# Performance work log

Measured on AMD Instinct MI355X. Metric: run time of the kernel, lower is better.

Reference implementation:

```python
import jax, jax.numpy as jnp
import numpy as np

LN_EPS = 1e-5      # torch nn.LayerNorm default
NORM_EPS = 1e-12   # torch F.normalize default
EPS = 1e-8         # loss eps


def layer_norm(x, gamma, beta):
    mu = x.mean(axis=-1, keepdims=True)
    var = x.var(axis=-1, keepdims=True)  # biased, matches torch LN
    return (x - mu) * jax.lax.rsqrt(var + LN_EPS) * gamma + beta


def l2norm(x):
    n = jnp.sqrt(jnp.sum(x * x, axis=-1, keepdims=True))
    return x / jnp.maximum(n, NORM_EPS)


def setup_inputs() -> dict:
    key = jax.random.key(0)
    k1, k2, k3 = jax.random.split(key, 3)
    N, B, L, D = 1024, 64, 197, 768
    text_features = jax.random.normal(k1, (N, D), dtype=jnp.float32)
    vision_tokens = jax.random.normal(k2, (B, L, D), dtype=jnp.float32)
    group_map = jnp.sort(jax.random.randint(k3, (N,), 0, B)).astype(jnp.int64)
    ln_gamma = jnp.ones((D,), dtype=jnp.float32)
    ln_beta = jnp.zeros((D,), dtype=jnp.float32)
    log_loss_temp = jnp.array([np.log(0.07)], dtype=jnp.float32)
    return {
        "text_features": text_features,
        "vision_tokens": vision_tokens,
        "group_map": group_map,
        "ln_gamma": ln_gamma,
        "ln_beta": ln_beta,
        "log_loss_temp": log_loss_temp,
    }


def reference(text_features, vision_tokens, group_map, ln_gamma, ln_beta, log_loss_temp):
    D = text_features.shape[-1]
    # shared LayerNorm on both modalities
    tf = layer_norm(text_features, ln_gamma, ln_beta)          # [N, D]
    vt = layer_norm(vision_tokens, ln_gamma, ln_beta)          # [B, L, D]

    # SimilarityLogit, sim_op='dot': scores / sqrt(D), softmax over tokens
    scores = jnp.einsum('nd,bld->bnl', tf, vt) / jnp.sqrt(jnp.float32(D))
    attn = jax.nn.softmax(scores, axis=-1)                     # [B, N, L]
    aggregated = jnp.einsum('bnl,bld->bnd', attn, vt)          # [B, N, D]

    qn = l2norm(tf)                                            # [N, D]
    an = l2norm(aggregated)                                    # [B, N, D]
    logits = jnp.einsum('nd,bnd->nb', qn, an)                  # [N, B] (== [B,N].T)

    # multi-positive NCE loss (row_sum=False, col_sum=False)
    temp = jnp.exp(log_loss_temp)[0]
    scaled = jnp.exp(logits / temp)                            # [N, B]
    N = scaled.shape[0]
    idx = jnp.arange(N)
    pos = scaled[idx, group_map]                               # [N]

    # row loss: pos / sum over images
    row_p = pos / (scaled.sum(axis=1) + EPS)
    row_loss = -jnp.log(row_p + EPS)

    # column loss: pos / (pos + sum of negatives in its column)
    neg_mask = jnp.ones_like(scaled).at[idx, group_map].set(0.0)
    sum_neg = (scaled * neg_mask).sum(axis=0)[group_map]       # [N]
    col_p = pos / (pos + sum_neg + EPS)
    col_loss = -jnp.log(col_p + EPS)

    return (row_loss.mean() + col_loss.mean()) / 2
```

## Files before the change

kernel.cpp:

```cpp
#include <hip/hip_runtime.h>
#include <hip/hip_bf16.h>
#include <math.h>

#define NN 1024
#define BB 64
#define LL 197
#define LP 256
#define LBV 13
#define DD 768

typedef __attribute__((ext_vector_type(8))) short short8;
typedef __attribute__((ext_vector_type(4))) float f32x4;

constexpr float LN_EPS = 1e-5f;
constexpr float NORM_EPS = 1e-12f;
constexpr float EPS = 1e-8f;

__device__ __forceinline__ float waveSum(float v) {
#pragma unroll
    for (int m = 32; m >= 1; m >>= 1) v += __shfl_xor(v, m, 64);
    return v;
}
__device__ __forceinline__ float grpSum(float v) {
#pragma unroll
    for (int m = 8; m >= 1; m >>= 1) v += __shfl_xor(v, m, 64);
    return v;
}
__device__ __forceinline__ float grpMax(float v) {
#pragma unroll
    for (int m = 8; m >= 1; m >>= 1) v = fmaxf(v, __shfl_xor(v, m, 64));
    return v;
}

__device__ __forceinline__ float bf2f(unsigned short u) {
    unsigned int x = ((unsigned int)u) << 16;
    return reinterpret_cast<float&>(x);
}

__device__ __forceinline__ void gl_lds16(const void* g, void* l) {
    __builtin_amdgcn_global_load_lds(
        (const __attribute__((address_space(1))) unsigned int*)g,
        (__attribute__((address_space(3))) unsigned int*)l, 16, 0, 0);
}

__device__ __forceinline__ void lite_barrier() {
    asm volatile("s_barrier" ::: "memory");
}

__global__ __launch_bounds__(256) void ln_kernel(
    const float* __restrict__ x, __hip_bfloat16* __restrict__ y,
    const float* __restrict__ gamma, const float* __restrict__ beta,
    float* __restrict__ qinv) {
    const int row = blockIdx.x;
    const int tid = threadIdx.x;
    const float* xr = x + (size_t)row * DD;

    float v[3];
    float s = 0.f, ss = 0.f;
#pragma unroll
    for (int c = 0; c < 3; c++) {
        float t = xr[tid + 256 * c];
        v[c] = t; s += t; ss += t * t;
    }
    __shared__ float red[8];
    s = waveSum(s); ss = waveSum(ss);
    const int w = tid >> 6;
    if ((tid & 63) == 0) { red[w] = s; red[4 + w] = ss; }
    __syncthreads();
    s = red[0] + red[1] + red[2] + red[3];
    ss = red[4] + red[5] + red[6] + red[7];
    const float mean = s * (1.f / DD);
    const float var = ss * (1.f / DD) - mean * mean;
    const float rs = rsqrtf(var + LN_EPS);

    float q = 0.f;
#pragma unroll
    for (int c = 0; c < 3; c++) {
        const int d = tid + 256 * c;
        float t = (v[c] - mean) * rs * gamma[d] + beta[d];
        __hip_bfloat16 hb = __float2bfloat16(t);
        y[((size_t)(d >> 5) * NN + row) * 32 + (d & 31)] = hb;
        float tb = __bfloat162float(hb);
        q += tb * tb;
    }
    __syncthreads();
    q = waveSum(q);
    if ((tid & 63) == 0) red[w] = q;
    __syncthreads();
    if (tid == 0) {
        float n2 = red[0] + red[1] + red[2] + red[3];
        qinv[row] = 1.f / fmaxf(sqrtf(n2), NORM_EPS);
    }
}

__global__ __launch_bounds__(256) void ln_vis_kernel(
    const float* __restrict__ x, __hip_bfloat16* __restrict__ y,
    const float* __restrict__ gamma, const float* __restrict__ beta) {
    const int id = blockIdx.x;
    const int xcd = id & 7;
    const int k = id >> 3;
    const int bhi = k >> 8;
    const int l = k & 255;
    const int b = xcd + 8 * bhi;
    const int tid = threadIdx.x;
    if (l >= LL) {
#pragma unroll
        for (int c = 0; c < 3; c++) {
            const int d = tid + 256 * c;
            y[(((size_t)b * 24 + (d >> 5)) * LP + l) * 32 + (d & 31)] = __float2bfloat16(0.f);
        }
        return;
    }
    const float* xr = x + ((size_t)b * LL + l) * DD;

    float v[3];
    float s = 0.f, ss = 0.f;
#pragma unroll
    for (int c = 0; c < 3; c++) {
        float t = xr[tid + 256 * c];
        v[c] = t; s += t; ss += t * t;
    }
    __shared__ float red[8];
    s = waveSum(s); ss = waveSum(ss);
    const int w = tid >> 6;
    if ((tid & 63) == 0) { red[w] = s; red[4 + w] = ss; }
    __syncthreads();
    s = red[0] + red[1] + red[2] + red[3];
    ss = red[4] + red[5] + red[6] + red[7];
    const float mean = s * (1.f / DD);
    const float var = ss * (1.f / DD) - mean * mean;
    const float rs = rsqrtf(var + LN_EPS);
#pragma unroll
    for (int c = 0; c < 3; c++) {
        const int d = tid + 256 * c;
        y[(((size_t)b * 24 + (d >> 5)) * LP + l) * 32 + (d & 31)] =
            __float2bfloat16((v[c] - mean) * rs * gamma[d] + beta[d]);
    }
}

__global__ __launch_bounds__(256, 2) void gram_kernel(
    const __hip_bfloat16* __restrict__ vt_t, __hip_bfloat16* __restrict__ G_t) {
    const int id = blockIdx.x;
    const int xcd = id & 7;
    const int k = id >> 3;
    const int bhi = k >> 3;
    const int rb = k & 7;
    const int b = xcd + 8 * bhi;
    const int n0 = rb * 32;
    const int tid = threadIdx.x, w = tid >> 6, lane = tid & 63;
    const int g = lane >> 4, c = lane & 15;
    const int gsw = (g ^ ((c ^ (c >> 2)) & 3)) * 16;

    __shared__ __align__(16) unsigned char smem[49152];
    const char* vtbc = (const char*)vt_t + (size_t)b * 24 * 16384;

#define GSTAGE(ks, bsel)                                                        \
    {                                                                           \
        const char* vsl_ = vtbc + (size_t)(ks) * 16384;                         \
        _Pragma("unroll")                                                       \
        for (int q_ = 0; q_ < 4; q_++) {                                        \
            const int o_ = q_ * 4096 + tid * 16;                                \
            const int r_ = o_ >> 6;                                             \
            const int sj_ = ((o_ >> 4) & 3) ^ ((r_ ^ (r_ >> 2)) & 3);           \
            gl_lds16(vsl_ + r_ * 64 + sj_ * 16,                                 \
                     smem + (bsel) * 16384 + q_ * 4096 + w * 1024);             \
        }                                                                       \
    }

    f32x4 acc[4][2];
#pragma unroll
    for (int i = 0; i < 4; i++)
#pragma unroll
        for (int nb = 0; nb < 2; nb++) acc[i][nb] = {0.f, 0.f, 0.f, 0.f};

    GSTAGE(0, 0);
    GSTAGE(1, 1);
    asm volatile("s_waitcnt vmcnt(4)" ::: "memory");
    lite_barrier();

    for (int ks = 0; ks < 24; ks++) {
        if (ks < 22) GSTAGE(ks + 2, (ks + 2) % 3);
        const unsigned char* vb = smem + (ks % 3) * 16384;
        short8 af[2], bf[4];
#pragma unroll
        for (int nb = 0; nb < 2; nb++)
            af[nb] = *(const short8*)(vb + (n0 + nb * 16 + c) * 64 + gsw);
#pragma unroll
        for (int i = 0; i < 4; i++)
            bf[i] = *(const short8*)(vb + ((w + 4 * i) * 16 + c) * 64 + gsw);
#pragma unroll
        for (int i = 0; i < 4; i++)
#pragma unroll
            for (int nb = 0; nb < 2; nb++)
                acc[i][nb] = __builtin_amdgcn_mfma_f32_16x16x32_bf16(
                    af[nb], bf[i], acc[i][nb], 0, 0, 0);
        if (ks < 22) asm volatile("s_waitcnt vmcnt(4)" ::: "memory");
        else         asm volatile("s_waitcnt vmcnt(0)" ::: "memory");
        lite_barrier();
    }
#undef GSTAGE

#pragma unroll
    for (int i = 0; i < 4; i++) {
        const int cw = w + 4 * i;
#pragma unroll
        for (int nb = 0; nb < 2; nb++)
#pragma unroll
            for (int r = 0; r < 4; r++)
                G_t[(((size_t)b * 8 + (cw >> 1)) * LP + n0 + nb * 16 + g * 4 + r) * 32 +
                    (cw & 1) * 16 + c] = __float2bfloat16(acc[i][nb][r]);
    }
}

__global__ __launch_bounds__(256, 3) void score_kernel(
    const __hip_bfloat16* __restrict__ tf_t, const __hip_bfloat16* __restrict__ vt_t,
    const float* __restrict__ qinv, __hip_bfloat16* __restrict__ P_t,
    float* __restrict__ numq) {
    const int id = blockIdx.x;
    const int xcd = id & 7;
    const int kk = id >> 3;
    const int bhi = kk >> 4;
    const int nt = kk & 15;
    const int b = xcd + 8 * bhi;
    const int n0 = nt * 64;
    const int tid = threadIdx.x, w = tid >> 6, lane = tid & 63;
    const int g = lane >> 4, c = lane & 15;
    const int gsw = (g ^ ((c ^ (c >> 2)) & 3)) * 16;

    __shared__ __align__(16) unsigned char smem[34816];
    float* mx = (float*)smem;
    float* sm = mx + 256;
    float* nm = sm + 256;

    const char* vtbc = (const char*)vt_t + (size_t)b * 24 * 16384;
    const char* tfc = (const char*)tf_t;

#define SSTAGE(ks, bsel)                                                        \
    {                                                                           \
        const char* vsl_ = vtbc + (size_t)(ks) * 16384;                         \
        const char* tsl_ = tfc + (size_t)(ks) * 65536 + (size_t)n0 * 64;        \
        _Pragma("unroll")                                                       \
        for (int q_ = 0; q_ < 3; q_++) {                                        \
            const int o_ = q_ * 4096 + tid * 16;                                \
            const int r_ = o_ >> 6;                                             \
            const int sj_ = ((o_ >> 4) & 3) ^ ((r_ ^ (r_ >> 2)) & 3);           \
            gl_lds16(vsl_ + r_ * 64 + sj_ * 16,                                 \
                     smem + (bsel) * 13312 + q_ * 4096 + w * 1024);             \
        }                                                                       \
        if (lane < 16) {                                                        \
            const int o_ = 12288 + (w * 16 + lane) * 16;                        \
            const int r_ = o_ >> 6;                                             \
            const int sj_ = ((o_ >> 4) & 3) ^ ((r_ ^ (r_ >> 2)) & 3);           \
            gl_lds16(vsl_ + r_ * 64 + sj_ * 16,                                 \
                     smem + (bsel) * 13312 + 12288 + w * 256);                  \
        }                                                                       \
        {                                                                       \
            const int o_ = tid * 16;                                            \
            const int r_ = o_ >> 6;                                             \
            const int sj_ = ((o_ >> 4) & 3) ^ ((r_ ^ (r_ >> 2)) & 3);           \
            gl_lds16(tsl_ + r_ * 64 + sj_ * 16,                                 \
                     smem + 26624 + (bsel) * 4096 + w * 1024);                  \
        }                                                                       \
    }

    f32x4 acc[4][4];
#pragma unroll
    for (int i = 0; i < 4; i++)
#pragma unroll
        for (int nb = 0; nb < 4; nb++) acc[i][nb] = {0.f, 0.f, 0.f, 0.f};

    SSTAGE(0, 0);
    SSTAGE(1, 1);
    asm volatile("s_waitcnt vmcnt(5)" ::: "memory");
    lite_barrier();

    for (int ks = 0; ks < 24; ks++) {
        const unsigned char* vb = smem + (ks & 1) * 13312;
        const unsigned char* tb = smem + 26624 + (ks & 1) * 4096;
        short8 af[4];
#pragma unroll
        for (int nb = 0; nb < 4; nb++)
            af[nb] = *(const short8*)(tb + (nb * 16 + c) * 64 + gsw);
#pragma unroll
        for (int i = 0; i < 4; i++) {
            const int lb = w + 4 * i;
            if (lb < LBV) {
                short8 bfv = *(const short8*)(vb + (lb * 16 + c) * 64 + gsw);
#pragma unroll
                for (int nb = 0; nb < 4; nb++)
                    acc[i][nb] = __builtin_amdgcn_mfma_f32_16x16x32_bf16(
                        af[nb], bfv, acc[i][nb], 0, 0, 0);
            }
        }
        lite_barrier();
        if (ks < 22) {
            SSTAGE(ks + 2, ks & 1);
            asm volatile("s_waitcnt vmcnt(5)" ::: "memory");
        } else {
            asm volatile("s_waitcnt vmcnt(0)" ::: "memory");
        }
        lite_barrier();
    }
#undef SSTAGE

    const float inv_sqrtD = 0.0360843918f;
    float mp[4][4];
#pragma unroll
    for (int nb = 0; nb < 4; nb++)
#pragma unroll
        for (int r = 0; r < 4; r++) mp[nb][r] = -1e30f;
#pragma unroll
    for (int i = 0; i < 4; i++) {
        const int l = (w + 4 * i) * 16 + c;
        if (l < LL) {
#pragma unroll
            for (int nb = 0; nb < 4; nb++)
#pragma unroll
                for (int r = 0; r < 4; r++) mp[nb][r] = fmaxf(mp[nb][r], acc[i][nb][r]);
        }
    }
#pragma unroll
    for (int nb = 0; nb < 4; nb++)
#pragma unroll
        for (int r = 0; r < 4; r++) mp[nb][r] = grpMax(mp[nb][r]);
    if (c == 0) {
#pragma unroll
        for (int nb = 0; nb < 4; nb++)
#pragma unroll
            for (int r = 0; r < 4; r++) mx[(nb * 16 + g * 4 + r) * 4 + w] = mp[nb][r];
    }
    __syncthreads();
    float mf[4][4];
#pragma unroll
    for (int nb = 0; nb < 4; nb++)
#pragma unroll
        for (int r = 0; r < 4; r++) {
            const int row = nb * 16 + g * 4 + r;
            mf[nb][r] = fmaxf(fmaxf(mx[row * 4 + 0], mx[row * 4 + 1]),
                              fmaxf(mx[row * 4 + 2], mx[row * 4 + 3]));
        }

    float sp[4][4], np[4][4];
#pragma unroll
    for (int nb = 0; nb < 4; nb++)
#pragma unroll
        for (int r = 0; r < 4; r++) { sp[nb][r] = 0.f; np[nb][r] = 0.f; }
#pragma unroll
    for (int i = 0; i < 4; i++) {
        const int l = (w + 4 * i) * 16 + c;
#pragma unroll
        for (int nb = 0; nb < 4; nb++)
#pragma unroll
            for (int r = 0; r < 4; r++) {
                const float raw = acc[i][nb][r];
                const float p = (l < LL) ? __expf((raw - mf[nb][r]) * inv_sqrtD) : 0.f;
                acc[i][nb][r] = p;
                sp[nb][r] += p;
                np[nb][r] += p * raw;
            }
    }
#pragma unroll
    for (int nb = 0; nb < 4; nb++)
#pragma unroll
        for (int r = 0; r < 4; r++) { sp[nb][r] = grpSum(sp[nb][r]); np[nb][r] = grpSum(np[nb][r]); }
    if (c == 0) {
#pragma unroll
        for (int nb = 0; nb < 4; nb++)
#pragma unroll
            for (int r = 0; r < 4; r++) {
                const int row = nb * 16 + g * 4 + r;
                sm[row * 4 + w] = sp[nb][r];
                nm[row * 4 + w] = np[nb][r];
            }
    }
    __syncthreads();

    float invs[4][4];
#pragma unroll
    for (int nb = 0; nb < 4; nb++)
#pragma unroll
        for (int r = 0; r < 4; r++) {
            const int row = nb * 16 + g * 4 + r;
            const float ssum = sm[row * 4 + 0] + sm[row * 4 + 1] + sm[row * 4 + 2] + sm[row * 4 + 3];
            invs[nb][r] = 1.f / ssum;
        }

#pragma unroll
    for (int i = 0; i < 4; i++) {
        const int lb = w + 4 * i;
#pragma unroll
        for (int nb = 0; nb < 4; nb++)
#pragma unroll
            for (int r = 0; r < 4; r++)
                P_t[(((size_t)b * 8 + (lb >> 1)) * NN + n0 + nb * 16 + g * 4 + r) * 32 +
                    (lb & 1) * 16 + c] = __float2bfloat16(acc[i][nb][r] * invs[nb][r]);
    }

    if (tid < 64) {
        const int row = tid;
        const int n = n0 + row;
        const float ssum = sm[row * 4 + 0] + sm[row * 4 + 1] + sm[row * 4 + 2] + sm[row * 4 + 3];
        const float nsum = nm[row * 4 + 0] + nm[row * 4 + 1] + nm[row * 4 + 2] + nm[row * 4 + 3];
        numq[(size_t)n * BB + b] = (nsum / ssum) * qinv[n];
    }
}

__global__ __launch_bounds__(256, 3) void den_kernel(
    const __hip_bfloat16* __restrict__ P_t, const __hip_bfloat16* __restrict__ G_t,
    const float* __restrict__ numq, float* __restrict__ logits) {
    const int id = blockIdx.x;
    const int xcd = id & 7;
    const int kk = id >> 3;
    const int bhi = kk >> 4;
    const int nt = kk & 15;
    const int b = xcd + 8 * bhi;
    const int n0 = nt * 64;
    const int tid = threadIdx.x, w = tid >> 6, lane = tid & 63;
    const int g = lane >> 4, c = lane & 15;
    const int gsw = (g ^ ((c ^ (c >> 2)) & 3)) * 16;

    __shared__ __align__(16) unsigned char smem[34816];
    float* mx = (float*)smem;

    const char* Gbc = (const char*)G_t + (size_t)b * 8 * 16384;
    const char* Pbc = (const char*)P_t + (size_t)b * 8 * 65536;

#define DSTAGE(ks, bsel)                                                        \
    {                                                                           \
        const char* vsl_ = Gbc + (size_t)(ks) * 16384;                          \
        const char* psl_ = Pbc + (size_t)(ks) * 65536 + (size_t)n0 * 64;        \
        _Pragma("unroll")                                                       \
        for (int q_ = 0; q_ < 3; q_++) {                                        \
            const int o_ = q_ * 4096 + tid * 16;                                \
            const int r_ = o_ >> 6;                                             \
            const int sj_ = ((o_ >> 4) & 3) ^ ((r_ ^ (r_ >> 2)) & 3);           \
            gl_lds16(vsl_ + r_ * 64 + sj_ * 16,                                 \
                     smem + (bsel) * 13312 + q_ * 4096 + w * 1024);             \
        }                                                                       \
        if (lane < 16) {                                                        \
            const int o_ = 12288 + (w * 16 + lane) * 16;                        \
            const int r_ = o_ >> 6;                                             \
            const int sj_ = ((o_ >> 4) & 3) ^ ((r_ ^ (r_ >> 2)) & 3);           \
            gl_lds16(vsl_ + r_ * 64 + sj_ * 16,                                 \
                     smem + (bsel) * 13312 + 12288 + w * 256);                  \
        }                                                                       \
        {                                                                       \
            const int o_ = tid * 16;                                            \
            const int r_ = o_ >> 6;                                             \
            const int sj_ = ((o_ >> 4) & 3) ^ ((r_ ^ (r_ >> 2)) & 3);           \
            gl_lds16(psl_ + r_ * 64 + sj_ * 16,                                 \
                     smem + 26624 + (bsel) * 4096 + w * 1024);                  \
        }                                                                       \
    }

    f32x4 acc[4][4];
#pragma unroll
    for (int i = 0; i < 4; i++)
#pragma unroll
        for (int nb = 0; nb < 4; nb++) acc[i][nb] = {0.f, 0.f, 0.f, 0.f};

    DSTAGE(0, 0);
    DSTAGE(1, 1);
    asm volatile("s_waitcnt vmcnt(5)" ::: "memory");
    lite_barrier();

    for (int ks = 0; ks < 7; ks++) {
        const unsigned char* vb = smem + (ks & 1) * 13312;
        const unsigned char* tb = smem + 26624 + (ks & 1) * 4096;
        short8 af[4];
#pragma unroll
        for (int nb = 0; nb < 4; nb++)
            af[nb] = *(const short8*)(tb + (nb * 16 + c) * 64 + gsw);
#pragma unroll
        for (int i = 0; i < 4; i++) {
            const int lb = w + 4 * i;
            if (lb < LBV) {
                short8 bfv = *(const short8*)(vb + (lb * 16 + c) * 64 + gsw);
#pragma unroll
                for (int nb = 0; nb < 4; nb++)
                    acc[i][nb] = __builtin_amdgcn_mfma_f32_16x16x32_bf16(
                        af[nb], bfv, acc[i][nb], 0, 0, 0);
            }
        }
        lite_barrier();
        if (ks < 5) {
            DSTAGE(ks + 2, ks & 1);
            asm volatile("s_waitcnt vmcnt(5)" ::: "memory");
        } else {
            asm volatile("s_waitcnt vmcnt(0)" ::: "memory");
        }
        lite_barrier();
    }
#undef DSTAGE

    const short* Pg = (const short*)P_t;
    float den[4][4];
#pragma unroll
    for (int nb = 0; nb < 4; nb++)
#pragma unroll
        for (int r = 0; r < 4; r++) den[nb][r] = 0.f;
#pragma unroll
    for (int i = 0; i < 4; i++) {
        const int lb = w + 4 * i;
        if (lb < LBV) {
#pragma unroll
            for (int nb = 0; nb < 4; nb++)
#pragma unroll
                for (int r = 0; r < 4; r++) {
                    const size_t pa = (((size_t)b * 8 + (lb >> 1)) * NN + n0 + nb * 16 + g * 4 + r) * 32 +
                                      (lb & 1) * 16 + c;
                    den[nb][r] += bf2f((unsigned short)Pg[pa]) * acc[i][nb][r];
                }
        }
    }

#pragma unroll
    for (int nb = 0; nb < 4; nb++)
#pragma unroll
        for (int r = 0; r < 4; r++) den[nb][r] = grpSum(den[nb][r]);
    __syncthreads();
    if (c == 0) {
#pragma unroll
        for (int nb = 0; nb < 4; nb++)
#pragma unroll
            for (int r = 0; r < 4; r++) mx[(nb * 16 + g * 4 + r) * 4 + w] = den[nb][r];
    }
    __syncthreads();
    if (tid < 64) {
        const int row = tid;
        const int n = n0 + row;
        const float dsum = mx[row * 4 + 0] + mx[row * 4 + 1] + mx[row * 4 + 2] + mx[row * 4 + 3];
        const float dn = fmaxf(sqrtf(fmaxf(dsum, 0.f)), NORM_EPS);
        logits[(size_t)n * BB + b] = numq[(size_t)n * BB + b] / dn;
    }
}

__global__ __launch_bounds__(64) void loss_row_kernel(
    const float* __restrict__ logits, const int* __restrict__ gm,
    const float* __restrict__ logtemp, float* __restrict__ scaled,
    float* __restrict__ posv, float* __restrict__ rowloss) {
    const int n = blockIdx.x;
    const int b = threadIdx.x;
    const float invtemp = 1.f / expf(logtemp[0]);
    const float e = expf(logits[(size_t)n * BB + b] * invtemp);
    scaled[(size_t)n * BB + b] = e;
    const float sum = waveSum(e);
    const int g = gm[n];
    const float pos = __shfl(e, g, 64);
    if (b == 0) {
        posv[n] = pos;
        rowloss[n] = -logf(pos / (sum + EPS) + EPS);
    }
}

__global__ __launch_bounds__(256) void colsum_kernel(
    const float* __restrict__ scaled, const int* __restrict__ gm,
    float* __restrict__ colsum, float* __restrict__ poscol) {
    const int b = blockIdx.x;
    const int tid = threadIdx.x;
    float s = 0.f, p = 0.f;
    for (int n = tid; n < NN; n += 256) {
        const float e = scaled[(size_t)n * BB + b];
        s += e;
        if (gm[n] == b) p += e;
    }
    s = waveSum(s); p = waveSum(p);
    __shared__ float red[8];
    const int w = tid >> 6;
    if ((tid & 63) == 0) { red[w] = s; red[4 + w] = p; }
    __syncthreads();
    if (tid == 0) {
        colsum[b] = red[0] + red[1] + red[2] + red[3];
        poscol[b] = red[4] + red[5] + red[6] + red[7];
    }
}

__global__ __launch_bounds__(1024) void final_kernel(
    const float* __restrict__ posv, const float* __restrict__ rowloss,
    const float* __restrict__ colsum, const float* __restrict__ poscol,
    const int* __restrict__ gm, float* __restrict__ out) {
    const int n = threadIdx.x;
    const int g = gm[n];
    const float pos = posv[n];
    const float sum_neg = colsum[g] - poscol[g];
    const float cl = -logf(pos / (pos + sum_neg + EPS) + EPS);
    float v = rowloss[n] + cl;
    v = waveSum(v);
    __shared__ float red[16];
    if ((n & 63) == 0) red[n >> 6] = v;
    __syncthreads();
    if (n == 0) {
        float s = 0.f;
#pragma unroll
        for (int i = 0; i < 16; i++) s += red[i];
        out[0] = s / (2.f * NN);
    }
}

extern "C" void kernel_launch(void* const* d_in, const int* in_sizes, int n_in,
                              void* d_out, int out_size, void* d_ws, size_t ws_size,
                              hipStream_t stream) {
    const float* text = (const float*)d_in[0];
    const float* vis = (const float*)d_in[1];
    const int* gm = (const int*)d_in[2];
    const float* gamma = (const float*)d_in[3];
    const float* beta = (const float*)d_in[4];
    const float* logtemp = (const float*)d_in[5];
    float* out = (float*)d_out;

    char* w = (char*)d_ws;
    __hip_bfloat16* tf_t = (__hip_bfloat16*)w;  w += (size_t)24 * NN * 32 * 2;
    __hip_bfloat16* vt_t = (__hip_bfloat16*)w;  w += (size_t)BB * 24 * LP * 32 * 2;
    __hip_bfloat16* G_t  = (__hip_bfloat16*)w;  w += (size_t)BB * 8 * LP * 32 * 2;
    __hip_bfloat16* P_t  = (__hip_bfloat16*)w;  w += (size_t)BB * 8 * NN * 32 * 2;
    float* qinv    = (float*)w;  w += (size_t)NN * 4;
    float* numq    = (float*)w;  w += (size_t)NN * BB * 4;
    float* logits  = (float*)w;  w += (size_t)NN * BB * 4;
    float* scaled  = (float*)w;  w += (size_t)NN * BB * 4;
    float* posv    = (float*)w;  w += (size_t)NN * 4;
    float* rowloss = (float*)w;  w += (size_t)NN * 4;
    float* colsum  = (float*)w;  w += (size_t)BB * 4;
    float* poscol  = (float*)w;  w += (size_t)BB * 4;

    ln_kernel<<<NN, 256, 0, stream>>>(text, tf_t, gamma, beta, qinv);
    ln_vis_kernel<<<BB * LP, 256, 0, stream>>>(vis, vt_t, gamma, beta);

    score_kernel<<<1024, 256, 0, stream>>>(tf_t, vt_t, qinv, P_t, numq);
    gram_kernel<<<512, 256, 0, stream>>>(vt_t, G_t);
    den_kernel<<<1024, 256, 0, stream>>>(P_t, G_t, numq, logits);

    loss_row_kernel<<<NN, 64, 0, stream>>>(logits, gm, logtemp, scaled, posv, rowloss);
    colsum_kernel<<<BB, 256, 0, stream>>>(scaled, gm, colsum, poscol);
    final_kernel<<<1, 1024, 0, stream>>>(posv, rowloss, colsum, poscol, gm, out);
}
```

Measured before the change: 113.0 us.

## Double score kernel N-tile to 128 rows with 512-thread blocks

Each score block now covers 128 text rows instead of 64, using 8 waves split into two row groups that share the same staged vision-token tile. This halves how often the per-image vision slab is reloaded from global memory and halves the block count. The trade-offs are larger LDS use per block, fewer blocks (512) for latency hiding, and coarser scheduling granularity.

New measurement: 109.6 us, median of 2. -3.0%, faster.

```diff
diff --git a/kernel.cpp b/kernel.cpp
--- a/kernel.cpp
+++ b/kernel.cpp
@@ -212,25 +212,26 @@
     }
 }
 
-__global__ __launch_bounds__(256, 3) void score_kernel(
+__global__ __launch_bounds__(512, 2) void score_kernel(
     const __hip_bfloat16* __restrict__ tf_t, const __hip_bfloat16* __restrict__ vt_t,
     const float* __restrict__ qinv, __hip_bfloat16* __restrict__ P_t,
     float* __restrict__ numq) {
     const int id = blockIdx.x;
     const int xcd = id & 7;
     const int kk = id >> 3;
-    const int bhi = kk >> 4;
-    const int nt = kk & 15;
+    const int bhi = kk >> 3;
+    const int nt = kk & 7;
     const int b = xcd + 8 * bhi;
-    const int n0 = nt * 64;
+    const int n0 = nt * 128;
     const int tid = threadIdx.x, w = tid >> 6, lane = tid & 63;
+    const int wn = w >> 2, wl = w & 3;
     const int g = lane >> 4, c = lane & 15;
     const int gsw = (g ^ ((c ^ (c >> 2)) & 3)) * 16;
 
-    __shared__ __align__(16) unsigned char smem[34816];
+    __shared__ __align__(16) unsigned char smem[49152];
     float* mx = (float*)smem;
-    float* sm = mx + 256;
-    float* nm = sm + 256;
+    float* sm = mx + 512;
+    float* nm = sm + 512;
 
     const char* vtbc = (const char*)vt_t + (size_t)b * 24 * 16384;
     const char* tfc = (const char*)tf_t;
@@ -240,26 +241,19 @@
         const char* vsl_ = vtbc + (size_t)(ks) * 16384;                         \
         const char* tsl_ = tfc + (size_t)(ks) * 65536 + (size_t)n0 * 64;        \
         _Pragma("unroll")                                                       \
-        for (int q_ = 0; q_ < 3; q_++) {                                        \
-            const int o_ = q_ * 4096 + tid * 16;                                \
+        for (int q_ = 0; q_ < 2; q_++) {                                        \
+            const int o_ = q_ * 8192 + tid * 16;                                \
             const int r_ = o_ >> 6;                                             \
             const int sj_ = ((o_ >> 4) & 3) ^ ((r_ ^ (r_ >> 2)) & 3);           \
             gl_lds16(vsl_ + r_ * 64 + sj_ * 16,                                 \
-                     smem + (bsel) * 13312 + q_ * 4096 + w * 1024);             \
-        }                                                                       \
-        if (lane < 16) {                                                        \
-            const int o_ = 12288 + (w * 16 + lane) * 16;                        \
-            const int r_ = o_ >> 6;                                             \
-            const int sj_ = ((o_ >> 4) & 3) ^ ((r_ ^ (r_ >> 2)) & 3);           \
-            gl_lds16(vsl_ + r_ * 64 + sj_ * 16,                                 \
-                     smem + (bsel) * 13312 + 12288 + w * 256);                  \
+                     smem + (bsel) * 16384 + q_ * 8192 + w * 1024);             \
         }                                                                       \
         {                                                                       \
             const int o_ = tid * 16;                                            \
             const int r_ = o_ >> 6;                                             \
             const int sj_ = ((o_ >> 4) & 3) ^ ((r_ ^ (r_ >> 2)) & 3);           \
             gl_lds16(tsl_ + r_ * 64 + sj_ * 16,                                 \
-                     smem + 26624 + (bsel) * 4096 + w * 1024);                  \
+                     smem + 32768 + (bsel) * 8192 + w * 1024);                  \
         }                                                                       \
     }
 
@@ -271,19 +265,19 @@
 
     SSTAGE(0, 0);
     SSTAGE(1, 1);
-    asm volatile("s_waitcnt vmcnt(5)" ::: "memory");
+    asm volatile("s_waitcnt vmcnt(3)" ::: "memory");
     lite_barrier();
 
     for (int ks = 0; ks < 24; ks++) {
-        const unsigned char* vb = smem + (ks & 1) * 13312;
-        const unsigned char* tb = smem + 26624 + (ks & 1) * 4096;
+        const unsigned char* vb = smem + (ks & 1) * 16384;
+        const unsigned char* tb = smem + 32768 + (ks & 1) * 8192;
         short8 af[4];
 #pragma unroll
         for (int nb = 0; nb < 4; nb++)
-            af[nb] = *(const short8*)(tb + (nb * 16 + c) * 64 + gsw);
+            af[nb] = *(const short8*)(tb + (wn * 64 + nb * 16 + c) * 64 + gsw);
 #pragma unroll
         for (int i = 0; i < 4; i++) {
-            const int lb = w + 4 * i;
+            const int lb = wl + 4 * i;
             if (lb < LBV) {
                 short8 bfv = *(const short8*)(vb + (lb * 16 + c) * 64 + gsw);
 #pragma unroll
@@ -295,7 +289,7 @@
         lite_barrier();
         if (ks < 22) {
             SSTAGE(ks + 2, ks & 1);
-            asm volatile("s_waitcnt vmcnt(5)" ::: "memory");
+            asm volatile("s_waitcnt vmcnt(3)" ::: "memory");
         } else {
             asm volatile("s_waitcnt vmcnt(0)" ::: "memory");
         }
@@ -311,7 +305,7 @@
         for (int r = 0; r < 4; r++) mp[nb][r] = -1e30f;
 #pragma unroll
     for (int i = 0; i < 4; i++) {
-        const int l = (w + 4 * i) * 16 + c;
+        const int l = (wl + 4 * i) * 16 + c;
         if (l < LL) {
 #pragma unroll
             for (int nb = 0; nb < 4; nb++)
@@ -327,7 +321,8 @@
 #pragma unroll
         for (int nb = 0; nb < 4; nb++)
 #pragma unroll
-            for (int r = 0; r < 4; r++) mx[(nb * 16 + g * 4 + r) * 4 + w] = mp[nb][r];
+            for (int r = 0; r < 4; r++)
+                mx[(wn * 64 + nb * 16 + g * 4 + r) * 4 + wl] = mp[nb][r];
     }
     __syncthreads();
     float mf[4][4];
@@ -335,7 +330,7 @@
     for (int nb = 0; nb < 4; nb++)
 #pragma unroll
         for (int r = 0; r < 4; r++) {
-            const int row = nb * 16 + g * 4 + r;
+            const int row = wn * 64 + nb * 16 + g * 4 + r;
             mf[nb][r] = fmaxf(fmaxf(mx[row * 4 + 0], mx[row * 4 + 1]),
                               fmaxf(mx[row * 4 + 2], mx[row * 4 + 3]));
         }
@@ -347,7 +342,7 @@
         for (int r = 0; r < 4; r++) { sp[nb][r] = 0.f; np[nb][r] = 0.f; }
 #pragma unroll
     for (int i = 0; i < 4; i++) {
-        const int l = (w + 4 * i) * 16 + c;
+        const int l = (wl + 4 * i) * 16 + c;
 #pragma unroll
         for (int nb = 0; nb < 4; nb++)
 #pragma unroll
@@ -368,9 +363,9 @@
         for (int nb = 0; nb < 4; nb++)
 #pragma unroll
             for (int r = 0; r < 4; r++) {
-                const int row = nb * 16 + g * 4 + r;
-                sm[row * 4 + w] = sp[nb][r];
-                nm[row * 4 + w] = np[nb][r];
+                const int row = wn * 64 + nb * 16 + g * 4 + r;
+                sm[row * 4 + wl] = sp[nb][r];
+                nm[row * 4 + wl] = np[nb][r];
             }
     }
     __syncthreads();
@@ -380,23 +375,23 @@
     for (int nb = 0; nb < 4; nb++)
 #pragma unroll
         for (int r = 0; r < 4; r++) {
-            const int row = nb * 16 + g * 4 + r;
+            const int row = wn * 64 + nb * 16 + g * 4 + r;
             const float ssum = sm[row * 4 + 0] + sm[row * 4 + 1] + sm[row * 4 + 2] + sm[row * 4 + 3];
             invs[nb][r] = 1.f / ssum;
         }
 
 #pragma unroll
     for (int i = 0; i < 4; i++) {
-        const int lb = w + 4 * i;
+        const int lb = wl + 4 * i;
 #pragma unroll
         for (int nb = 0; nb < 4; nb++)
 #pragma unroll
             for (int r = 0; r < 4; r++)
-                P_t[(((size_t)b * 8 + (lb >> 1)) * NN + n0 + nb * 16 + g * 4 + r) * 32 +
+                P_t[(((size_t)b * 8 + (lb >> 1)) * NN + n0 + wn * 64 + nb * 16 + g * 4 + r) * 32 +
                     (lb & 1) * 16 + c] = __float2bfloat16(acc[i][nb][r] * invs[nb][r]);
     }
 
-    if (tid < 64) {
+    if (tid < 128) {
         const int row = tid;
         const int n = n0 + row;
         const float ssum = sm[row * 4 + 0] + sm[row * 4 + 1] + sm[row * 4 + 2] + sm[row * 4 + 3];
@@ -625,7 +620,7 @@
     ln_kernel<<<NN, 256, 0, stream>>>(text, tf_t, gamma, beta, qinv);
     ln_vis_kernel<<<BB * LP, 256, 0, stream>>>(vis, vt_t, gamma, beta);
 
-    score_kernel<<<1024, 256, 0, stream>>>(tf_t, vt_t, qinv, P_t, numq);
+    score_kernel<<<512, 512, 0, stream>>>(tf_t, vt_t, qinv, P_t, numq);
     gram_kernel<<<512, 256, 0, stream>>>(vt_t, G_t);
     den_kernel<<<1024, 256, 0, stream>>>(P_t, G_t, numq, logits);
 
```
